# Performance work log

Measured on AMD Instinct MI355X. Metric: run time of the kernel, lower is better.

Reference implementation:

```python
import jax, jax.numpy as jnp
import numpy as np

H = 128          # h_dim
N_NODES = 100000
N_EDGES = 1600000
N_GRAPHS = 256
EPS_BN = 1e-5


def setup_inputs() -> dict:
    key = jax.random.key(0)
    ks = jax.random.split(key, 12)
    x = jax.random.normal(ks[0], (N_NODES, 4), dtype=jnp.float32)
    edge_index = jax.random.randint(ks[1], (2, N_EDGES), 0, N_NODES, dtype=jnp.int64)
    batch = jnp.sort(jax.random.randint(ks[2], (N_NODES,), 0, N_GRAPHS, dtype=jnp.int64))
    # Linear weights (xavier-ish scale), stored as [in, out]
    W1 = jax.random.normal(ks[3], (4, H), dtype=jnp.float32) * (1.0 / np.sqrt(4))
    W2 = jax.random.normal(ks[4], (H, H), dtype=jnp.float32) * (1.0 / np.sqrt(H))
    W3 = jax.random.normal(ks[5], (H, H), dtype=jnp.float32) * (1.0 / np.sqrt(H))
    Wfc = jax.random.normal(ks[6], (H, 1), dtype=jnp.float32) * (1.0 / np.sqrt(H))
    def bn_params(k):
        k1, k2, k3, k4 = jax.random.split(k, 4)
        gamma = 1.0 + 0.1 * jax.random.normal(k1, (H,), dtype=jnp.float32)
        beta = 0.1 * jax.random.normal(k2, (H,), dtype=jnp.float32)
        mean = 0.1 * jax.random.normal(k3, (H,), dtype=jnp.float32)
        var = 1.0 + 0.1 * jax.random.uniform(k4, (H,), dtype=jnp.float32)
        return gamma, beta, mean, var
    g1, b1, m1, v1 = bn_params(ks[7])
    g2, b2, m2, v2 = bn_params(ks[8])
    g3, b3, m3, v3 = bn_params(ks[9])
    return {
        "x": x, "edge_index": edge_index, "batch": batch,
        "W1": W1, "g1": g1, "b1": b1, "m1": m1, "v1": v1,
        "W2": W2, "g2": g2, "b2": b2, "m2": m2, "v2": v2,
        "W3": W3, "g3": g3, "b3": b3, "m3": m3, "v3": v3,
        "Wfc": Wfc,
    }


def _gin_layer(h, src, dst, W, gamma, beta, mean, var):
    # GINConv with eps=0: mlp(x + sum_{j in N(i)} x_j)
    aggr = jax.ops.segment_sum(h[src], dst, num_segments=N_NODES)
    z = (h + aggr) @ W                                  # Linear(bias=False)
    z = (z - mean) * (gamma / jnp.sqrt(var + EPS_BN)) + beta  # BatchNorm1d (eval)
    return jax.nn.relu(z)


def reference(x, edge_index, batch,
              W1, g1, b1, m1, v1,
              W2, g2, b2, m2, v2,
              W3, g3, b3, m3, v3,
              Wfc):
    src, dst = edge_index[0], edge_index[1]
    h = _gin_layer(x, src, dst, W1, g1, b1, m1, v1)
    h = _gin_layer(h, src, dst, W2, g2, b2, m2, v2)
    h = _gin_layer(h, src, dst, W3, g3, b3, m3, v3)
    # dropout: identity in eval mode
    sums = jax.ops.segment_sum(h, batch, num_segments=N_GRAPHS)      # [G, H]
    cnts = jax.ops.segment_sum(jnp.ones((N_NODES, 1), h.dtype), batch,
                               num_segments=N_GRAPHS)                # [G, 1]
    pooled = sums / jnp.maximum(cnts, 1.0)
    return jax.nn.sigmoid(pooled @ Wfc)                               # [G, 1]
```

## Files before the change

### kernel.cpp

```cpp
#include <hip/hip_runtime.h>
#include <hip/hip_fp8.h>
#include <math.h>

#define N_NODES 100000
#define N_EDGES 1600000
#define N_GRAPHS 256
#define H 128
#define EPS_BN 1e-5f
#define ELLW 64

#define PSZ 256
#define PSH 8
#define P_PART 391
#define BLD_NBLK 200
#define EPT 32
#define EPB_A (256 * EPT)

typedef unsigned int uint;
typedef unsigned short ushort;
typedef __attribute__((ext_vector_type(8))) short bf16x8;
typedef __attribute__((ext_vector_type(4))) float f32x4;
typedef __attribute__((ext_vector_type(2))) float f32x2;
typedef __attribute__((ext_vector_type(4))) int i32x4;
typedef __attribute__((ext_vector_type(2))) int i32x2;

__device__ __forceinline__ uint f2bf_bits(float x) {
    uint u = __float_as_uint(x);
    return (u + 0x7fffu + ((u >> 16) & 1u)) >> 16;
}
__device__ __forceinline__ uint pack_bf2(float a, float b) {
    return f2bf_bits(a) | (f2bf_bits(b) << 16);
}
__device__ __forceinline__ float bf_lo(uint p) { return __uint_as_float(p << 16); }
__device__ __forceinline__ float bf_hi(uint p) { return __uint_as_float(p & 0xffff0000u); }

__device__ __forceinline__ unsigned char f32_to_fp8(float x) {
#if __has_builtin(__builtin_amdgcn_cvt_pk_fp8_f32)
    int v = __builtin_amdgcn_cvt_pk_fp8_f32(x, 0.0f, 0, false);
    return (unsigned char)(v & 0xff);
#else
    __hip_fp8_e4m3 q(x);
    return (unsigned char)q.__x;
#endif
}
__device__ __forceinline__ f32x4 fp8x4_to_f32x4(uint v) {
    f32x4 r;
#if __has_builtin(__builtin_amdgcn_cvt_pk_f32_fp8)
    f32x2 lo = __builtin_amdgcn_cvt_pk_f32_fp8((int)v, false);
    f32x2 hi = __builtin_amdgcn_cvt_pk_f32_fp8((int)v, true);
    r.x = lo.x; r.y = lo.y; r.z = hi.x; r.w = hi.y;
#else
    __hip_fp8_e4m3 a, b, c, d;
    a.__x = (unsigned char)(v & 0xff);
    b.__x = (unsigned char)((v >> 8) & 0xff);
    c.__x = (unsigned char)((v >> 16) & 0xff);
    d.__x = (unsigned char)((v >> 24) & 0xff);
    r.x = (float)a; r.y = (float)b; r.z = (float)c; r.w = (float)d;
#endif
    return r;
}

__global__ __launch_bounds__(256) void k_hist(const int* __restrict__ dst,
                                              int* __restrict__ hist,
                                              const int* __restrict__ batch,
                                              int* __restrict__ gstart,
                                              const float* __restrict__ W2,
                                              ushort* __restrict__ Wpk2,
                                              const float* __restrict__ W3,
                                              ushort* __restrict__ Wpk3,
                                              float* __restrict__ Gz) {
    __shared__ int h[P_PART];
    int b = blockIdx.x;
    if (b < BLD_NBLK) {
        for (int i = threadIdx.x; i < P_PART; i += 256) h[i] = 0;
        __syncthreads();
        int base = b * EPB_A + threadIdx.x * EPT;
        #pragma unroll
        for (int j = 0; j < EPT / 4; j++) {
            int e = base + j * 4;
            if (e + 4 <= N_EDGES) {
                i32x4 d = __builtin_nontemporal_load((const i32x4*)&dst[e]);
                atomicAdd(&h[d.x >> PSH], 1);
                atomicAdd(&h[d.y >> PSH], 1);
                atomicAdd(&h[d.z >> PSH], 1);
                atomicAdd(&h[d.w >> PSH], 1);
            }
        }
        __syncthreads();
        for (int i = threadIdx.x; i < P_PART; i += 256)
            hist[b * P_PART + i] = h[i];
        return;
    }
    if (b < 592) {
        int n = (b - 200) * 256 + threadIdx.x;
        if (n >= N_NODES) return;
        int g = batch[n];
        int gp = (n == 0) ? -1 : batch[n - 1];
        for (int gr = gp + 1; gr <= g; gr++) gstart[gr] = n;
        if (n == N_NODES - 1) {
            for (int gr = g + 1; gr <= N_GRAPHS; gr++) gstart[gr] = N_NODES;
        }
        return;
    }
    if (b >= 608) {
        if (threadIdx.x < N_GRAPHS) Gz[threadIdx.x] = 0.0f;
        return;
    }
    const float* W = (b < 600) ? W2 : W3;
    ushort* Wpk = (b < 600) ? Wpk2 : Wpk3;
    int t = ((b < 600) ? (b - 592) : (b - 600)) * 256 + threadIdx.x;
    int lane = t & 63, nt = (t >> 6) & 7, kt = t >> 9;
    int n = nt * 16 + (lane & 15);
    int kbase = kt * 32 + (lane >> 4) * 8;
    ushort v[8];
    #pragma unroll
    for (int j = 0; j < 8; j++)
        v[j] = (ushort)f2bf_bits(W[(size_t)(kbase + j) * H + n]);
    uint4 pk;
    pk.x = (uint)v[0] | ((uint)v[1] << 16);
    pk.y = (uint)v[2] | ((uint)v[3] << 16);
    pk.z = (uint)v[4] | ((uint)v[5] << 16);
    pk.w = (uint)v[6] | ((uint)v[7] << 16);
    *(uint4*)&Wpk[(size_t)t * 8] = pk;
}

__global__ __launch_bounds__(256) void k_scan_a(const int* __restrict__ hist,
                                                int* __restrict__ offs,
                                                int* __restrict__ tot) {
    __shared__ int lds[256];
    int p = blockIdx.x;
    int t = threadIdx.x;
    int v = (t < BLD_NBLK) ? hist[t * P_PART + p] : 0;
    lds[t] = v;
    __syncthreads();
    for (int off = 1; off < 256; off <<= 1) {
        int tmp = (t >= off) ? lds[t - off] : 0;
        __syncthreads();
        lds[t] += tmp;
        __syncthreads();
    }
    if (t < BLD_NBLK) offs[t * P_PART + p] = lds[t] - v;
    if (t == 255) tot[p] = lds[255];
}

__global__ void k_scan_b(const int* __restrict__ tot, int* __restrict__ parr) {
    __shared__ int lds[512];
    int p = threadIdx.x;
    int v = (p < P_PART) ? tot[p] : 0;
    lds[p] = v;
    __syncthreads();
    for (int off = 1; off < 512; off <<= 1) {
        int tmp = (p >= off) ? lds[p - off] : 0;
        __syncthreads();
        lds[p] += tmp;
        __syncthreads();
    }
    if (p < P_PART) parr[p] = lds[p] - v;
    if (p == 0) parr[P_PART] = N_EDGES;
}

__global__ __launch_bounds__(256) void k_scatter(const int* __restrict__ src,
                                                 const int* __restrict__ dst,
                                                 const int* __restrict__ offs,
                                                 const int* __restrict__ parr,
                                                 i32x2* __restrict__ ebuf) {
    __shared__ int lofs[P_PART];
    for (int i = threadIdx.x; i < P_PART; i += 256)
        lofs[i] = offs[blockIdx.x * P_PART + i] + parr[i];
    __syncthreads();
    int base = blockIdx.x * EPB_A + threadIdx.x * EPT;
    #pragma unroll
    for (int j = 0; j < EPT / 4; j++) {
        int e = base + j * 4;
        if (e + 4 <= N_EDGES) {
            i32x4 d = __builtin_nontemporal_load((const i32x4*)&dst[e]);
            i32x4 s = __builtin_nontemporal_load((const i32x4*)&src[e]);
            #pragma unroll
            for (int k = 0; k < 4; k++) {
                int dk = (k == 0) ? d.x : (k == 1) ? d.y : (k == 2) ? d.z : d.w;
                int sk = (k == 0) ? s.x : (k == 1) ? s.y : (k == 2) ? s.z : s.w;
                int pos = atomicAdd(&lofs[dk >> PSH], 1);
                i32x2 sd; sd.x = sk; sd.y = dk;
                ebuf[pos] = sd;
            }
        }
    }
}

__global__ __launch_bounds__(256) void k_build(const i32x2* __restrict__ ebuf,
                                               const int* __restrict__ parr,
                                               int* __restrict__ cnt,
                                               int* __restrict__ ell) {
    __shared__ int lc[PSZ];
    int p = blockIdx.x;
    for (int i = threadIdx.x; i < PSZ; i += 256) lc[i] = 0;
    __syncthreads();
    int e0 = parr[p], e1 = parr[p + 1];
    for (int i = e0 + threadIdx.x; i < e1; i += 256) {
        i32x2 sd = ebuf[i];
        int d = sd.y;
        int slot = atomicAdd(&lc[d & (PSZ - 1)], 1);
        if (slot < ELLW) ell[(size_t)d * ELLW + slot] = sd.x;
    }
    __syncthreads();
    int nb = p * PSZ;
    for (int i = threadIdx.x; i < PSZ; i += 256) {
        int n = nb + i;
        if (n < N_NODES) cnt[n] = lc[i];
    }
}

__global__ __launch_bounds__(256) void k_layer1(
    const float* __restrict__ x, const int* __restrict__ cnt,
    const int* __restrict__ ell, const float* __restrict__ W1,
    const float* __restrict__ gamma, const float* __restrict__ beta,
    const float* __restrict__ mean, const float* __restrict__ var,
    uint* __restrict__ Hf8) {
    __shared__ float scs[128], shs[128];
    int tid = threadIdx.x;
    if (tid < 128) {
        float sc = gamma[tid] * rsqrtf(var[tid] + EPS_BN);
        scs[tid] = sc;
        shs[tid] = beta[tid] - mean[tid] * sc;
    }
    __syncthreads();
    int lane = tid & 63, wave = tid >> 6;
    int sub = lane >> 4, m = lane & 15;
    int n = blockIdx.x * 16 + wave * 4 + sub;
    if (n >= N_NODES) return;
    int cn = cnt[n]; if (cn > ELLW) cn = ELLW;
    const int* row = &ell[(size_t)n * ELLW];
    float4 acc = {0.f, 0.f, 0.f, 0.f};
    for (int e = m; e < cn; e += 16) {
        float4 v = *(const float4*)&x[(size_t)row[e] * 4];
        acc.x += v.x; acc.y += v.y; acc.z += v.z; acc.w += v.w;
    }
    #pragma unroll
    for (int off = 8; off > 0; off >>= 1) {
        acc.x += __shfl_down(acc.x, off, 16);
        acc.y += __shfl_down(acc.y, off, 16);
        acc.z += __shfl_down(acc.z, off, 16);
        acc.w += __shfl_down(acc.w, off, 16);
    }
    int src = lane & 48;
    float4 xs = *(const float4*)&x[(size_t)n * 4];
    float uu[4];
    uu[0] = __shfl(acc.x, src, 64) + xs.x;
    uu[1] = __shfl(acc.y, src, 64) + xs.y;
    uu[2] = __shfl(acc.z, src, 64) + xs.z;
    uu[3] = __shfl(acc.w, src, 64) + xs.w;
    int j0 = m * 8;
    float z[8] = {0.f, 0.f, 0.f, 0.f, 0.f, 0.f, 0.f, 0.f};
    #pragma unroll
    for (int k = 0; k < 4; k++) {
        float4 wa = *(const float4*)&W1[k * H + j0];
        float4 wb = *(const float4*)&W1[k * H + j0 + 4];
        z[0] += uu[k] * wa.x; z[1] += uu[k] * wa.y;
        z[2] += uu[k] * wa.z; z[3] += uu[k] * wa.w;
        z[4] += uu[k] * wb.x; z[5] += uu[k] * wb.y;
        z[6] += uu[k] * wb.z; z[7] += uu[k] * wb.w;
    }
    #pragma unroll
    for (int i = 0; i < 8; i++)
        z[i] = fmaxf(z[i] * scs[j0 + i] + shs[j0 + i], 0.0f);
    uint2 q;
    q.x = (uint)f32_to_fp8(z[0]) | ((uint)f32_to_fp8(z[1]) << 8)
        | ((uint)f32_to_fp8(z[2]) << 16) | ((uint)f32_to_fp8(z[3]) << 24);
    q.y = (uint)f32_to_fp8(z[4]) | ((uint)f32_to_fp8(z[5]) << 8)
        | ((uint)f32_to_fp8(z[6]) << 16) | ((uint)f32_to_fp8(z[7]) << 24);
    *(uint2*)&Hf8[(size_t)n * 32 + m * 2] = q;
}

__global__ __launch_bounds__(256) void k_aggr128(
    const uint* __restrict__ Hf8, const int* __restrict__ cnt,
    const int* __restrict__ ell, uint* __restrict__ Ubf) {
    int t = blockIdx.x * 256 + threadIdx.x;
    int n = t >> 6, lane = t & 63;
    if (n >= N_NODES) return;
    int half = lane >> 5, c4 = lane & 31;
    float a0 = 0.f, a1 = 0.f, a2 = 0.f, a3 = 0.f;
    int cn = cnt[n]; if (cn > ELLW) cn = ELLW;
    const int* row = &ell[(size_t)n * ELLW];
    int e = half;
    for (; e + 14 < cn; e += 16) {
        int s0 = row[e + 0], s1 = row[e + 2], s2 = row[e + 4], s3 = row[e + 6];
        int s4 = row[e + 8], s5 = row[e + 10], s6 = row[e + 12], s7 = row[e + 14];
        uint p0 = Hf8[(size_t)s0 * 32 + c4];
        uint p1 = Hf8[(size_t)s1 * 32 + c4];
        uint p2 = Hf8[(size_t)s2 * 32 + c4];
        uint p3 = Hf8[(size_t)s3 * 32 + c4];
        uint p4 = Hf8[(size_t)s4 * 32 + c4];
        uint p5 = Hf8[(size_t)s5 * 32 + c4];
        uint p6 = Hf8[(size_t)s6 * 32 + c4];
        uint p7 = Hf8[(size_t)s7 * 32 + c4];
        f32x4 f0 = fp8x4_to_f32x4(p0), f1 = fp8x4_to_f32x4(p1);
        f32x4 f2 = fp8x4_to_f32x4(p2), f3 = fp8x4_to_f32x4(p3);
        f32x4 f4 = fp8x4_to_f32x4(p4), f5 = fp8x4_to_f32x4(p5);
        f32x4 f6 = fp8x4_to_f32x4(p6), f7 = fp8x4_to_f32x4(p7);
        a0 += (f0.x + f1.x + f2.x + f3.x) + (f4.x + f5.x + f6.x + f7.x);
        a1 += (f0.y + f1.y + f2.y + f3.y) + (f4.y + f5.y + f6.y + f7.y);
        a2 += (f0.z + f1.z + f2.z + f3.z) + (f4.z + f5.z + f6.z + f7.z);
        a3 += (f0.w + f1.w + f2.w + f3.w) + (f4.w + f5.w + f6.w + f7.w);
    }
    for (; e + 6 < cn; e += 8) {
        int s0 = row[e + 0], s1 = row[e + 2], s2 = row[e + 4], s3 = row[e + 6];
        uint p0 = Hf8[(size_t)s0 * 32 + c4];
        uint p1 = Hf8[(size_t)s1 * 32 + c4];
        uint p2 = Hf8[(size_t)s2 * 32 + c4];
        uint p3 = Hf8[(size_t)s3 * 32 + c4];
        f32x4 f0 = fp8x4_to_f32x4(p0), f1 = fp8x4_to_f32x4(p1);
        f32x4 f2 = fp8x4_to_f32x4(p2), f3 = fp8x4_to_f32x4(p3);
        a0 += f0.x + f1.x + f2.x + f3.x;
        a1 += f0.y + f1.y + f2.y + f3.y;
        a2 += f0.z + f1.z + f2.z + f3.z;
        a3 += f0.w + f1.w + f2.w + f3.w;
    }
    for (; e < cn; e += 2) {
        f32x4 f = fp8x4_to_f32x4(Hf8[(size_t)row[e] * 32 + c4]);
        a0 += f.x; a1 += f.y; a2 += f.z; a3 += f.w;
    }
    a0 += __shfl_down(a0, 32, 64);
    a1 += __shfl_down(a1, 32, 64);
    a2 += __shfl_down(a2, 32, 64);
    a3 += __shfl_down(a3, 32, 64);
    if (half == 0) {
        f32x4 sf = fp8x4_to_f32x4(Hf8[(size_t)n * 32 + c4]);
        a0 += sf.x; a1 += sf.y; a2 += sf.z; a3 += sf.w;
        uint2 ov; ov.x = pack_bf2(a0, a1); ov.y = pack_bf2(a2, a3);
        *(uint2*)&Ubf[(size_t)n * 64 + c4 * 2] = ov;
    }
}

__global__ __launch_bounds__(256) void k_gemm_mfma(
    const uint* __restrict__ Ubf, const uint* __restrict__ Wpk,
    const float* __restrict__ gamma, const float* __restrict__ beta,
    const float* __restrict__ mean, const float* __restrict__ var,
    unsigned char* __restrict__ Hf8,
    const int* __restrict__ batch, const float* __restrict__ Wfc,
    float* __restrict__ Gz, int mode) {
    __shared__ uint lds_u[64 * 68];
    __shared__ float wfc[128];
    __shared__ int bb[64];
    __shared__ float sblk[64];
    int tid = threadIdx.x;
    int row0 = blockIdx.x * 64;
    if (mode == 2) {
        if (tid < 128) wfc[tid] = Wfc[tid];
        if (tid < 64) {
            int rr = row0 + tid;
            bb[tid] = (rr < N_NODES) ? batch[rr] : -1;
        }
    }
    #pragma unroll
    for (int it = 0; it < 4; it++) {
        int r = it * 16 + (tid >> 4);
        int c = (tid & 15) * 4;
        int gr = row0 + r; if (gr >= N_NODES) gr = N_NODES - 1;
        uint4 v = *(const uint4*)&Ubf[(size_t)gr * 64 + c];
        *(uint4*)&lds_u[r * 68 + c] = v;
    }
    __syncthreads();

    int wave = tid >> 6, lane = tid & 63;
    int m = lane & 15, quad = lane >> 4;
    bf16x8 a[4];
    #pragma unroll
    for (int kt = 0; kt < 4; kt++)
        a[kt] = *(const bf16x8*)&lds_u[(wave * 16 + m) * 68 + kt * 16 + quad * 4];

    f32x4 acc[8];
    #pragma unroll
    for (int nt = 0; nt < 8; nt++) acc[nt] = (f32x4){0.f, 0.f, 0.f, 0.f};

    #pragma unroll
    for (int nt = 0; nt < 8; nt++) {
        #pragma unroll
        for (int kt = 0; kt < 4; kt++) {
            bf16x8 b = *(const bf16x8*)&Wpk[((size_t)(kt * 8 + nt) * 64 + lane) * 4];
            acc[nt] = __builtin_amdgcn_mfma_f32_16x16x32_bf16(a[kt], b, acc[nt], 0, 0, 0);
        }
    }

    if (mode == 1) {
        #pragma unroll
        for (int nt = 0; nt < 8; nt++) {
            int col = nt * 16 + m;
            float sc = gamma[col] * rsqrtf(var[col] + EPS_BN);
            float sh = beta[col] - mean[col] * sc;
            #pragma unroll
            for (int r = 0; r < 4; r++) {
                int row = row0 + wave * 16 + quad * 4 + r;
                if (row < N_NODES) {
                    float z = fmaxf(acc[nt][r] * sc + sh, 0.0f);
                    Hf8[(size_t)row * 128 + col] = f32_to_fp8(z);
                }
            }
        }
    } else {
        float pr[4] = {0.f, 0.f, 0.f, 0.f};
        #pragma unroll
        for (int nt = 0; nt < 8; nt++) {
            int col = nt * 16 + m;
            float sc = gamma[col] * rsqrtf(var[col] + EPS_BN);
            float sh = beta[col] - mean[col] * sc;
            float wf = wfc[col];
            #pragma unroll
            for (int r = 0; r < 4; r++) {
                float z = fmaxf(acc[nt][r] * sc + sh, 0.0f);
                pr[r] += z * wf;
            }
        }
        #pragma unroll
        for (int r = 0; r < 4; r++) {
            float p = pr[r];
            p += __shfl_down(p, 8, 16);
            p += __shfl_down(p, 4, 16);
            p += __shfl_down(p, 2, 16);
            p += __shfl_down(p, 1, 16);
            if (m == 0) sblk[wave * 16 + quad * 4 + r] = p;
        }
        __syncthreads();
        if (tid == 0) {
            int i = 0;
            while (i < 64 && row0 + i < N_NODES) {
                int g = bb[i];
                float s = 0.0f;
                while (i < 64 && row0 + i < N_NODES && bb[i] == g) {
                    s += sblk[i]; i++;
                }
                atomicAdd(&Gz[g], s);
            }
        }
    }
}

__global__ void k_fc(const float* __restrict__ Gz, const int* __restrict__ gstart,
                     float* __restrict__ out) {
    int g = threadIdx.x;
    if (g < N_GRAPHS) {
        int c = gstart[g + 1] - gstart[g];
        float z = Gz[g] / fmaxf((float)c, 1.0f);
        out[g] = 1.0f / (1.0f + expf(-z));
    }
}

extern "C" void kernel_launch(void* const* d_in, const int* in_sizes, int n_in,
                              void* d_out, int out_size, void* d_ws, size_t ws_size,
                              hipStream_t stream) {
    const float* x     = (const float*)d_in[0];
    const int*   ei    = (const int*)d_in[1];
    const int*   batch = (const int*)d_in[2];
    const float* W1    = (const float*)d_in[3];
    const float* g1    = (const float*)d_in[4];
    const float* b1    = (const float*)d_in[5];
    const float* m1    = (const float*)d_in[6];
    const float* v1    = (const float*)d_in[7];
    const float* W2    = (const float*)d_in[8];
    const float* g2    = (const float*)d_in[9];
    const float* b2    = (const float*)d_in[10];
    const float* m2    = (const float*)d_in[11];
    const float* v2    = (const float*)d_in[12];
    const float* W3    = (const float*)d_in[13];
    const float* g3    = (const float*)d_in[14];
    const float* b3    = (const float*)d_in[15];
    const float* m3    = (const float*)d_in[16];
    const float* v3    = (const float*)d_in[17];
    const float* Wfc   = (const float*)d_in[18];
    float* out = (float*)d_out;

    const int* srcp = ei;
    const int* dstp = ei + N_EDGES;

    uint* Ubf  = (uint*)d_ws;
    uint* Hf8u = Ubf + (size_t)N_NODES * 64;
    int* cnt   = (int*)(Hf8u + (size_t)N_NODES * 32);
    int* ell   = cnt + N_NODES;
    int* gstart = ell + (size_t)N_NODES * ELLW;
    ushort* Wpk2 = (ushort*)(gstart + 260);
    ushort* Wpk3 = Wpk2 + 16384;
    int* hist  = (int*)(Wpk3 + 16384);
    int* offs  = hist + BLD_NBLK * P_PART;
    int* parr  = offs + BLD_NBLK * P_PART;
    int* tot   = parr + 400;
    float* Gz  = (float*)(tot + 400);
    i32x2* ebuf = (i32x2*)Ubf;

    k_hist<<<609, 256, 0, stream>>>(dstp, hist, batch, gstart, W2, Wpk2, W3, Wpk3, Gz);
    k_scan_a<<<P_PART, 256, 0, stream>>>(hist, offs, tot);
    k_scan_b<<<1, 512, 0, stream>>>(tot, parr);
    k_scatter<<<BLD_NBLK, 256, 0, stream>>>(srcp, dstp, offs, parr, ebuf);
    k_build<<<P_PART, 256, 0, stream>>>(ebuf, parr, cnt, ell);

    k_layer1<<<(N_NODES + 15) / 16, 256, 0, stream>>>(
        x, cnt, ell, W1, g1, b1, m1, v1, Hf8u);
    k_aggr128<<<(N_NODES * 64 + 255) / 256, 256, 0, stream>>>(Hf8u, cnt, ell, Ubf);
    k_gemm_mfma<<<(N_NODES + 63) / 64, 256, 0, stream>>>(
        Ubf, (const uint*)Wpk2, g2, b2, m2, v2, (unsigned char*)Hf8u,
        batch, Wfc, Gz, 1);
    k_aggr128<<<(N_NODES * 64 + 255) / 256, 256, 0, stream>>>(Hf8u, cnt, ell, Ubf);
    k_gemm_mfma<<<(N_NODES + 63) / 64, 256, 0, stream>>>(
        Ubf, (const uint*)Wpk3, g3, b3, m3, v3, (unsigned char*)Hf8u,
        batch, Wfc, Gz, 2);
    k_fc<<<1, 256, 0, stream>>>(Gz, gstart, out);
}
```

Baseline: 306.4 us.

## Fuse neighbor aggregation into MFMA GEMM kernel with ping-pong fp8 buffers

```diff
diff --git a/kernel.cpp b/kernel.cpp
--- a/kernel.cpp
+++ b/kernel.cpp
@@ -31,8 +31,6 @@
 __device__ __forceinline__ uint pack_bf2(float a, float b) {
     return f2bf_bits(a) | (f2bf_bits(b) << 16);
 }
-__device__ __forceinline__ float bf_lo(uint p) { return __uint_as_float(p << 16); }
-__device__ __forceinline__ float bf_hi(uint p) { return __uint_as_float(p & 0xffff0000u); }
 
 __device__ __forceinline__ unsigned char f32_to_fp8(float x) {
 #if __has_builtin(__builtin_amdgcn_cvt_pk_fp8_f32)
@@ -68,7 +66,8 @@
                                               ushort* __restrict__ Wpk2,
                                               const float* __restrict__ W3,
                                               ushort* __restrict__ Wpk3,
-                                              float* __restrict__ Gz) {
+                                              float* __restrict__ Gz,
+                                              uint* __restrict__ HfApad) {
     __shared__ int h[P_PART];
     int b = blockIdx.x;
     if (b < BLD_NBLK) {
@@ -104,6 +103,7 @@
     }
     if (b >= 608) {
         if (threadIdx.x < N_GRAPHS) Gz[threadIdx.x] = 0.0f;
+        if (threadIdx.x < 32) HfApad[threadIdx.x] = 0u;
         return;
     }
     const float* W = (b < 600) ? W2 : W3;
@@ -215,9 +215,10 @@
     const int* __restrict__ ell, const float* __restrict__ W1,
     const float* __restrict__ gamma, const float* __restrict__ beta,
     const float* __restrict__ mean, const float* __restrict__ var,
-    uint* __restrict__ Hf8) {
+    uint* __restrict__ Hf8, uint* __restrict__ HfBpad) {
     __shared__ float scs[128], shs[128];
     int tid = threadIdx.x;
+    if (blockIdx.x == 0 && tid < 32) HfBpad[tid] = 0u;
     if (tid < 128) {
         float sc = gamma[tid] * rsqrtf(var[tid] + EPS_BN);
         scs[tid] = sc;
@@ -271,74 +272,14 @@
     *(uint2*)&Hf8[(size_t)n * 32 + m * 2] = q;
 }
 
-__global__ __launch_bounds__(256) void k_aggr128(
-    const uint* __restrict__ Hf8, const int* __restrict__ cnt,
-    const int* __restrict__ ell, uint* __restrict__ Ubf) {
-    int t = blockIdx.x * 256 + threadIdx.x;
-    int n = t >> 6, lane = t & 63;
-    if (n >= N_NODES) return;
-    int half = lane >> 5, c4 = lane & 31;
-    float a0 = 0.f, a1 = 0.f, a2 = 0.f, a3 = 0.f;
-    int cn = cnt[n]; if (cn > ELLW) cn = ELLW;
-    const int* row = &ell[(size_t)n * ELLW];
-    int e = half;
-    for (; e + 14 < cn; e += 16) {
-        int s0 = row[e + 0], s1 = row[e + 2], s2 = row[e + 4], s3 = row[e + 6];
-        int s4 = row[e + 8], s5 = row[e + 10], s6 = row[e + 12], s7 = row[e + 14];
-        uint p0 = Hf8[(size_t)s0 * 32 + c4];
-        uint p1 = Hf8[(size_t)s1 * 32 + c4];
-        uint p2 = Hf8[(size_t)s2 * 32 + c4];
-        uint p3 = Hf8[(size_t)s3 * 32 + c4];
-        uint p4 = Hf8[(size_t)s4 * 32 + c4];
-        uint p5 = Hf8[(size_t)s5 * 32 + c4];
-        uint p6 = Hf8[(size_t)s6 * 32 + c4];
-        uint p7 = Hf8[(size_t)s7 * 32 + c4];
-        f32x4 f0 = fp8x4_to_f32x4(p0), f1 = fp8x4_to_f32x4(p1);
-        f32x4 f2 = fp8x4_to_f32x4(p2), f3 = fp8x4_to_f32x4(p3);
-        f32x4 f4 = fp8x4_to_f32x4(p4), f5 = fp8x4_to_f32x4(p5);
-        f32x4 f6 = fp8x4_to_f32x4(p6), f7 = fp8x4_to_f32x4(p7);
-        a0 += (f0.x + f1.x + f2.x + f3.x) + (f4.x + f5.x + f6.x + f7.x);
-        a1 += (f0.y + f1.y + f2.y + f3.y) + (f4.y + f5.y + f6.y + f7.y);
-        a2 += (f0.z + f1.z + f2.z + f3.z) + (f4.z + f5.z + f6.z + f7.z);
-        a3 += (f0.w + f1.w + f2.w + f3.w) + (f4.w + f5.w + f6.w + f7.w);
-    }
-    for (; e + 6 < cn; e += 8) {
-        int s0 = row[e + 0], s1 = row[e + 2], s2 = row[e + 4], s3 = row[e + 6];
-        uint p0 = Hf8[(size_t)s0 * 32 + c4];
-        uint p1 = Hf8[(size_t)s1 * 32 + c4];
-        uint p2 = Hf8[(size_t)s2 * 32 + c4];
-        uint p3 = Hf8[(size_t)s3 * 32 + c4];
-        f32x4 f0 = fp8x4_to_f32x4(p0), f1 = fp8x4_to_f32x4(p1);
-        f32x4 f2 = fp8x4_to_f32x4(p2), f3 = fp8x4_to_f32x4(p3);
-        a0 += f0.x + f1.x + f2.x + f3.x;
-        a1 += f0.y + f1.y + f2.y + f3.y;
-        a2 += f0.z + f1.z + f2.z + f3.z;
-        a3 += f0.w + f1.w + f2.w + f3.w;
-    }
-    for (; e < cn; e += 2) {
-        f32x4 f = fp8x4_to_f32x4(Hf8[(size_t)row[e] * 32 + c4]);
-        a0 += f.x; a1 += f.y; a2 += f.z; a3 += f.w;
-    }
-    a0 += __shfl_down(a0, 32, 64);
-    a1 += __shfl_down(a1, 32, 64);
-    a2 += __shfl_down(a2, 32, 64);
-    a3 += __shfl_down(a3, 32, 64);
-    if (half == 0) {
-        f32x4 sf = fp8x4_to_f32x4(Hf8[(size_t)n * 32 + c4]);
-        a0 += sf.x; a1 += sf.y; a2 += sf.z; a3 += sf.w;
-        uint2 ov; ov.x = pack_bf2(a0, a1); ov.y = pack_bf2(a2, a3);
-        *(uint2*)&Ubf[(size_t)n * 64 + c4 * 2] = ov;
-    }
-}
-
-__global__ __launch_bounds__(256) void k_gemm_mfma(
-    const uint* __restrict__ Ubf, const uint* __restrict__ Wpk,
+__global__ __launch_bounds__(256) void k_aggr_gemm(
+    const uint* __restrict__ Hin, const int* __restrict__ cnt,
+    const int* __restrict__ ell, const uint* __restrict__ Wpk,
     const float* __restrict__ gamma, const float* __restrict__ beta,
     const float* __restrict__ mean, const float* __restrict__ var,
-    unsigned char* __restrict__ Hf8,
+    unsigned char* __restrict__ Hout,
     const int* __restrict__ batch, const float* __restrict__ Wfc,
     float* __restrict__ Gz, int mode) {
-    __shared__ uint lds_u[64 * 68];
     __shared__ float wfc[128];
     __shared__ int bb[64];
     __shared__ float sblk[64];
@@ -351,22 +292,76 @@
             bb[tid] = (rr < N_NODES) ? batch[rr] : -1;
         }
     }
-    #pragma unroll
-    for (int it = 0; it < 4; it++) {
-        int r = it * 16 + (tid >> 4);
-        int c = (tid & 15) * 4;
-        int gr = row0 + r; if (gr >= N_NODES) gr = N_NODES - 1;
-        uint4 v = *(const uint4*)&Ubf[(size_t)gr * 64 + c];
-        *(uint4*)&lds_u[r * 68 + c] = v;
-    }
-    __syncthreads();
-
     int wave = tid >> 6, lane = tid & 63;
     int m = lane & 15, quad = lane >> 4;
+    int n = row0 + wave * 16 + m;
+    bool valid = (n < N_NODES);
+    int nc = valid ? n : 0;
+    int cn = valid ? cnt[n] : 0;
+    if (cn > ELLW) cn = ELLW;
+    int cn4 = (cn + 3) & ~3;
+    int wmax = cn4;
+    #pragma unroll
+    for (int off = 1; off < 16; off <<= 1)
+        wmax = max(wmax, __shfl_xor(wmax, off, 16));
+
+    const uint* selfrow = Hin + (size_t)nc * 32 + quad * 2;
+    uint2 sp0 = *(const uint2*)(selfrow);
+    uint2 sp1 = *(const uint2*)(selfrow + 8);
+    uint2 sp2 = *(const uint2*)(selfrow + 16);
+    uint2 sp3 = *(const uint2*)(selfrow + 24);
+
+    f32x4 fa0 = {0.f,0.f,0.f,0.f}, fb0 = {0.f,0.f,0.f,0.f};
+    f32x4 fa1 = {0.f,0.f,0.f,0.f}, fb1 = {0.f,0.f,0.f,0.f};
+    f32x4 fa2 = {0.f,0.f,0.f,0.f}, fb2 = {0.f,0.f,0.f,0.f};
+    f32x4 fa3 = {0.f,0.f,0.f,0.f}, fb3 = {0.f,0.f,0.f,0.f};
+
+    const int* rowp = ell + (size_t)nc * ELLW;
+    i32x4 id4 = *(const i32x4*)rowp;
+    for (int e = 0; e < wmax; e += 4) {
+        i32x4 nxt = *(const i32x4*)(rowp + ((e + 4) & (ELLW - 1)));
+        if (e < cn4) {
+            #pragma unroll
+            for (int j = 0; j < 4; j++) {
+                int s = (j == 0) ? id4.x : (j == 1) ? id4.y
+                      : (j == 2) ? id4.z : id4.w;
+                if (e + j >= cn) s = N_NODES;
+                const uint* gp = Hin + (size_t)s * 32 + quad * 2;
+                uint2 p0 = *(const uint2*)(gp);
+                uint2 p1 = *(const uint2*)(gp + 8);
+                uint2 p2 = *(const uint2*)(gp + 16);
+                uint2 p3 = *(const uint2*)(gp + 24);
+                fa0 += fp8x4_to_f32x4(p0.x); fb0 += fp8x4_to_f32x4(p0.y);
+                fa1 += fp8x4_to_f32x4(p1.x); fb1 += fp8x4_to_f32x4(p1.y);
+                fa2 += fp8x4_to_f32x4(p2.x); fb2 += fp8x4_to_f32x4(p2.y);
+                fa3 += fp8x4_to_f32x4(p3.x); fb3 += fp8x4_to_f32x4(p3.y);
+            }
+        }
+        id4 = nxt;
+    }
+    if (valid) {
+        fa0 += fp8x4_to_f32x4(sp0.x); fb0 += fp8x4_to_f32x4(sp0.y);
+        fa1 += fp8x4_to_f32x4(sp1.x); fb1 += fp8x4_to_f32x4(sp1.y);
+        fa2 += fp8x4_to_f32x4(sp2.x); fb2 += fp8x4_to_f32x4(sp2.y);
+        fa3 += fp8x4_to_f32x4(sp3.x); fb3 += fp8x4_to_f32x4(sp3.y);
+    }
+
+    union AB { uint4 u; bf16x8 v; };
     bf16x8 a[4];
-    #pragma unroll
-    for (int kt = 0; kt < 4; kt++)
-        a[kt] = *(const bf16x8*)&lds_u[(wave * 16 + m) * 68 + kt * 16 + quad * 4];
+    {
+        AB t0; t0.u = make_uint4(pack_bf2(fa0.x, fa0.y), pack_bf2(fa0.z, fa0.w),
+                                 pack_bf2(fb0.x, fb0.y), pack_bf2(fb0.z, fb0.w));
+        a[0] = t0.v;
+        AB t1; t1.u = make_uint4(pack_bf2(fa1.x, fa1.y), pack_bf2(fa1.z, fa1.w),
+                                 pack_bf2(fb1.x, fb1.y), pack_bf2(fb1.z, fb1.w));
+        a[1] = t1.v;
+        AB t2; t2.u = make_uint4(pack_bf2(fa2.x, fa2.y), pack_bf2(fa2.z, fa2.w),
+                                 pack_bf2(fb2.x, fb2.y), pack_bf2(fb2.z, fb2.w));
+        a[2] = t2.v;
+        AB t3; t3.u = make_uint4(pack_bf2(fa3.x, fa3.y), pack_bf2(fa3.z, fa3.w),
+                                 pack_bf2(fb3.x, fb3.y), pack_bf2(fb3.z, fb3.w));
+        a[3] = t3.v;
+    }
 
     f32x4 acc[8];
     #pragma unroll
@@ -392,7 +387,7 @@
                 int row = row0 + wave * 16 + quad * 4 + r;
                 if (row < N_NODES) {
                     float z = fmaxf(acc[nt][r] * sc + sh, 0.0f);
-                    Hf8[(size_t)row * 128 + col] = f32_to_fp8(z);
+                    Hout[(size_t)row * 128 + col] = f32_to_fp8(z);
                 }
             }
         }
@@ -471,9 +466,9 @@
     const int* srcp = ei;
     const int* dstp = ei + N_EDGES;
 
-    uint* Ubf  = (uint*)d_ws;
-    uint* Hf8u = Ubf + (size_t)N_NODES * 64;
-    int* cnt   = (int*)(Hf8u + (size_t)N_NODES * 32);
+    uint* HfB  = (uint*)d_ws;
+    uint* HfA  = HfB + (size_t)N_NODES * 64;
+    int* cnt   = (int*)(HfA + (size_t)N_NODES * 32 + 32);
     int* ell   = cnt + N_NODES;
     int* gstart = ell + (size_t)N_NODES * ELLW;
     ushort* Wpk2 = (ushort*)(gstart + 260);
@@ -483,23 +478,24 @@
     int* parr  = offs + BLD_NBLK * P_PART;
     int* tot   = parr + 400;
     float* Gz  = (float*)(tot + 400);
-    i32x2* ebuf = (i32x2*)Ubf;
-
-    k_hist<<<609, 256, 0, stream>>>(dstp, hist, batch, gstart, W2, Wpk2, W3, Wpk3, Gz);
+    i32x2* ebuf = (i32x2*)HfB;
+    uint* HfApad = HfA + (size_t)N_NODES * 32;
+    uint* HfBpad = HfB + (size_t)N_NODES * 32;
+
+    k_hist<<<609, 256, 0, stream>>>(dstp, hist, batch, gstart, W2, Wpk2, W3, Wpk3,
+                                    Gz, HfApad);
     k_scan_a<<<P_PART, 256, 0, stream>>>(hist, offs, tot);
     k_scan_b<<<1, 512, 0, stream>>>(tot, parr);
     k_scatter<<<BLD_NBLK, 256, 0, stream>>>(srcp, dstp, offs, parr, ebuf);
     k_build<<<P_PART, 256, 0, stream>>>(ebuf, parr, cnt, ell);
 
     k_layer1<<<(N_NODES + 15) / 16, 256, 0, stream>>>(
-        x, cnt, ell, W1, g1, b1, m1, v1, Hf8u);
-    k_aggr128<<<(N_NODES * 64 + 255) / 256, 256, 0, stream>>>(Hf8u, cnt, ell, Ubf);
-    k_gemm_mfma<<<(N_NODES + 63) / 64, 256, 0, stream>>>(
-        Ubf, (const uint*)Wpk2, g2, b2, m2, v2, (unsigned char*)Hf8u,
-        batch, Wfc, Gz, 1);
-    k_aggr128<<<(N_NODES * 64 + 255) / 256, 256, 0, stream>>>(Hf8u, cnt, ell, Ubf);
-    k_gemm_mfma<<<(N_NODES + 63) / 64, 256, 0, stream>>>(
-        Ubf, (const uint*)Wpk3, g3, b3, m3, v3, (unsigned char*)Hf8u,
-        batch, Wfc, Gz, 2);
+        x, cnt, ell, W1, g1, b1, m1, v1, HfA, HfBpad);
+    k_aggr_gemm<<<(N_NODES + 63) / 64, 256, 0, stream>>>(
+        HfA, cnt, ell, (const uint*)Wpk2, g2, b2, m2, v2,
+        (unsigned char*)HfB, batch, Wfc, Gz, 1);
+    k_aggr_gemm<<<(N_NODES + 63) / 64, 256, 0, stream>>>(
+        HfB, cnt, ell, (const uint*)Wpk3, g3, b3, m3, v3,
+        (unsigned char*)HfA, batch, Wfc, Gz, 2);
     k_fc<<<1, 256, 0, stream>>>(Gz, gstart, out);
 }
```

New measurement: 328.7 us. 7.3% more time.

## Pad ELL rows to sentinel zero node and vectorize fp8 neighbor gathers

Applied to the files above, without the earlier changes.

```diff
diff --git a/kernel.cpp b/kernel.cpp
--- a/kernel.cpp
+++ b/kernel.cpp
@@ -31,8 +31,6 @@
 __device__ __forceinline__ uint pack_bf2(float a, float b) {
     return f2bf_bits(a) | (f2bf_bits(b) << 16);
 }
-__device__ __forceinline__ float bf_lo(uint p) { return __uint_as_float(p << 16); }
-__device__ __forceinline__ float bf_hi(uint p) { return __uint_as_float(p & 0xffff0000u); }
 
 __device__ __forceinline__ unsigned char f32_to_fp8(float x) {
 #if __has_builtin(__builtin_amdgcn_cvt_pk_fp8_f32)
@@ -68,7 +66,8 @@
                                               ushort* __restrict__ Wpk2,
                                               const float* __restrict__ W3,
                                               ushort* __restrict__ Wpk3,
-                                              float* __restrict__ Gz) {
+                                              float* __restrict__ Gz,
+                                              uint* __restrict__ Hf8pad) {
     __shared__ int h[P_PART];
     int b = blockIdx.x;
     if (b < BLD_NBLK) {
@@ -104,6 +103,7 @@
     }
     if (b >= 608) {
         if (threadIdx.x < N_GRAPHS) Gz[threadIdx.x] = 0.0f;
+        if (threadIdx.x < 32) Hf8pad[threadIdx.x] = 0u;
         return;
     }
     const float* W = (b < 600) ? W2 : W3;
@@ -206,7 +206,15 @@
     int nb = p * PSZ;
     for (int i = threadIdx.x; i < PSZ; i += 256) {
         int n = nb + i;
-        if (n < N_NODES) cnt[n] = lc[i];
+        if (n < N_NODES) {
+            int c = lc[i];
+            cnt[n] = c;
+            int cc = (c < ELLW) ? c : ELLW;
+            int cp = (cc + 15) & ~15;
+            if (cp > ELLW) cp = ELLW;
+            for (int slot = cc; slot < cp; slot++)
+                ell[(size_t)n * ELLW + slot] = N_NODES;
+        }
     }
 }
 
@@ -277,57 +285,54 @@
     int t = blockIdx.x * 256 + threadIdx.x;
     int n = t >> 6, lane = t & 63;
     if (n >= N_NODES) return;
-    int half = lane >> 5, c4 = lane & 31;
-    float a0 = 0.f, a1 = 0.f, a2 = 0.f, a3 = 0.f;
+    int g = lane >> 4, c8 = lane & 15;
+    const int* row = &ell[(size_t)n * ELLW];
+    i32x4 id = *(const i32x4*)(row + 4 * g);
+    uint2 sp = {0u, 0u};
+    if (g == 0) sp = *(const uint2*)&Hf8[(size_t)n * 32 + c8 * 2];
     int cn = cnt[n]; if (cn > ELLW) cn = ELLW;
-    const int* row = &ell[(size_t)n * ELLW];
-    int e = half;
-    for (; e + 14 < cn; e += 16) {
-        int s0 = row[e + 0], s1 = row[e + 2], s2 = row[e + 4], s3 = row[e + 6];
-        int s4 = row[e + 8], s5 = row[e + 10], s6 = row[e + 12], s7 = row[e + 14];
-        uint p0 = Hf8[(size_t)s0 * 32 + c4];
-        uint p1 = Hf8[(size_t)s1 * 32 + c4];
-        uint p2 = Hf8[(size_t)s2 * 32 + c4];
-        uint p3 = Hf8[(size_t)s3 * 32 + c4];
-        uint p4 = Hf8[(size_t)s4 * 32 + c4];
-        uint p5 = Hf8[(size_t)s5 * 32 + c4];
-        uint p6 = Hf8[(size_t)s6 * 32 + c4];
-        uint p7 = Hf8[(size_t)s7 * 32 + c4];
-        f32x4 f0 = fp8x4_to_f32x4(p0), f1 = fp8x4_to_f32x4(p1);
-        f32x4 f2 = fp8x4_to_f32x4(p2), f3 = fp8x4_to_f32x4(p3);
-        f32x4 f4 = fp8x4_to_f32x4(p4), f5 = fp8x4_to_f32x4(p5);
-        f32x4 f6 = fp8x4_to_f32x4(p6), f7 = fp8x4_to_f32x4(p7);
-        a0 += (f0.x + f1.x + f2.x + f3.x) + (f4.x + f5.x + f6.x + f7.x);
-        a1 += (f0.y + f1.y + f2.y + f3.y) + (f4.y + f5.y + f6.y + f7.y);
-        a2 += (f0.z + f1.z + f2.z + f3.z) + (f4.z + f5.z + f6.z + f7.z);
-        a3 += (f0.w + f1.w + f2.w + f3.w) + (f4.w + f5.w + f6.w + f7.w);
-    }
-    for (; e + 6 < cn; e += 8) {
-        int s0 = row[e + 0], s1 = row[e + 2], s2 = row[e + 4], s3 = row[e + 6];
-        uint p0 = Hf8[(size_t)s0 * 32 + c4];
-        uint p1 = Hf8[(size_t)s1 * 32 + c4];
-        uint p2 = Hf8[(size_t)s2 * 32 + c4];
-        uint p3 = Hf8[(size_t)s3 * 32 + c4];
-        f32x4 f0 = fp8x4_to_f32x4(p0), f1 = fp8x4_to_f32x4(p1);
-        f32x4 f2 = fp8x4_to_f32x4(p2), f3 = fp8x4_to_f32x4(p3);
-        a0 += f0.x + f1.x + f2.x + f3.x;
-        a1 += f0.y + f1.y + f2.y + f3.y;
-        a2 += f0.z + f1.z + f2.z + f3.z;
-        a3 += f0.w + f1.w + f2.w + f3.w;
-    }
-    for (; e < cn; e += 2) {
-        f32x4 f = fp8x4_to_f32x4(Hf8[(size_t)row[e] * 32 + c4]);
-        a0 += f.x; a1 += f.y; a2 += f.z; a3 += f.w;
-    }
-    a0 += __shfl_down(a0, 32, 64);
-    a1 += __shfl_down(a1, 32, 64);
-    a2 += __shfl_down(a2, 32, 64);
-    a3 += __shfl_down(a3, 32, 64);
-    if (half == 0) {
-        f32x4 sf = fp8x4_to_f32x4(Hf8[(size_t)n * 32 + c4]);
-        a0 += sf.x; a1 += sf.y; a2 += sf.z; a3 += sf.w;
-        uint2 ov; ov.x = pack_bf2(a0, a1); ov.y = pack_bf2(a2, a3);
-        *(uint2*)&Ubf[(size_t)n * 64 + c4 * 2] = ov;
+    int cnp = (cn + 15) & ~15; if (cnp > ELLW) cnp = ELLW;
+
+    f32x4 A = {0.f, 0.f, 0.f, 0.f};
+    f32x4 B = {0.f, 0.f, 0.f, 0.f};
+    for (int e = 0; e < cnp; e += 16) {
+        i32x4 idn = id;
+        if (e + 16 < cnp) idn = *(const i32x4*)(row + e + 16 + 4 * g);
+        int s0 = id.x, s1 = id.y, s2 = id.z, s3 = id.w;
+        uint2 p0 = *(const uint2*)&Hf8[(size_t)s0 * 32 + c8 * 2];
+        uint2 p1 = *(const uint2*)&Hf8[(size_t)s1 * 32 + c8 * 2];
+        uint2 p2 = *(const uint2*)&Hf8[(size_t)s2 * 32 + c8 * 2];
+        uint2 p3 = *(const uint2*)&Hf8[(size_t)s3 * 32 + c8 * 2];
+        f32x4 l0 = fp8x4_to_f32x4(p0.x), h0 = fp8x4_to_f32x4(p0.y);
+        f32x4 l1 = fp8x4_to_f32x4(p1.x), h1 = fp8x4_to_f32x4(p1.y);
+        f32x4 l2 = fp8x4_to_f32x4(p2.x), h2 = fp8x4_to_f32x4(p2.y);
+        f32x4 l3 = fp8x4_to_f32x4(p3.x), h3 = fp8x4_to_f32x4(p3.y);
+        A += (l0 + l1) + (l2 + l3);
+        B += (h0 + h1) + (h2 + h3);
+        id = idn;
+    }
+    if (g == 0) {
+        A += fp8x4_to_f32x4(sp.x);
+        B += fp8x4_to_f32x4(sp.y);
+    }
+    #pragma unroll
+    for (int off = 32; off >= 16; off >>= 1) {
+        A.x += __shfl_down(A.x, off, 64);
+        A.y += __shfl_down(A.y, off, 64);
+        A.z += __shfl_down(A.z, off, 64);
+        A.w += __shfl_down(A.w, off, 64);
+        B.x += __shfl_down(B.x, off, 64);
+        B.y += __shfl_down(B.y, off, 64);
+        B.z += __shfl_down(B.z, off, 64);
+        B.w += __shfl_down(B.w, off, 64);
+    }
+    if (g == 0) {
+        uint4 ov;
+        ov.x = pack_bf2(A.x, A.y);
+        ov.y = pack_bf2(A.z, A.w);
+        ov.z = pack_bf2(B.x, B.y);
+        ov.w = pack_bf2(B.z, B.w);
+        *(uint4*)&Ubf[(size_t)n * 64 + c8 * 4] = ov;
     }
 }
 
@@ -473,7 +478,7 @@
 
     uint* Ubf  = (uint*)d_ws;
     uint* Hf8u = Ubf + (size_t)N_NODES * 64;
-    int* cnt   = (int*)(Hf8u + (size_t)N_NODES * 32);
+    int* cnt   = (int*)(Hf8u + (size_t)N_NODES * 32 + 32);
     int* ell   = cnt + N_NODES;
     int* gstart = ell + (size_t)N_NODES * ELLW;
     ushort* Wpk2 = (ushort*)(gstart + 260);
@@ -484,8 +489,10 @@
     int* tot   = parr + 400;
     float* Gz  = (float*)(tot + 400);
     i32x2* ebuf = (i32x2*)Ubf;
-
-    k_hist<<<609, 256, 0, stream>>>(dstp, hist, batch, gstart, W2, Wpk2, W3, Wpk3, Gz);
+    uint* Hf8pad = Hf8u + (size_t)N_NODES * 32;
+
+    k_hist<<<609, 256, 0, stream>>>(dstp, hist, batch, gstart, W2, Wpk2, W3, Wpk3,
+                                    Gz, Hf8pad);
     k_scan_a<<<P_PART, 256, 0, stream>>>(hist, offs, tot);
     k_scan_b<<<1, 512, 0, stream>>>(tot, parr);
     k_scatter<<<BLD_NBLK, 256, 0, stream>>>(srcp, dstp, offs, parr, ebuf);
```

New measurement: 278.0 us. 9.3% less time.
